# Performance work log

Measured on AMD Instinct MI355X. Metric: run time of the kernel, lower is better.

The kernel has to match this reference:

```python
import jax, jax.numpy as jnp
import numpy as np

B, S, D, H = 4, 2048, 768, 8
HD = D // H
EPS = 1e-5
NEG = -1e9


def setup_inputs() -> dict:
    key = jax.random.key(0)
    ks = jax.random.split(key, 12)
    s = 1.0 / np.sqrt(D)
    inp = {
        "hidden_states": jax.random.normal(ks[0], (B, S, D), dtype=jnp.float32),
        "anchor_mask": jax.random.bernoulli(ks[1], 0.5, (B, S)),
        "ln_g": jnp.ones((D,), jnp.float32),
        "ln_b": jnp.zeros((D,), jnp.float32),
        "Wq": jax.random.uniform(ks[2], (D, D), jnp.float32, -s, s),
        "bq": jax.random.uniform(ks[3], (D,), jnp.float32, -s, s),
        "Wk": jax.random.uniform(ks[4], (D, D), jnp.float32, -s, s),
        "bk": jax.random.uniform(ks[5], (D,), jnp.float32, -s, s),
        "Wv": jax.random.uniform(ks[6], (D, D), jnp.float32, -s, s),
        "bv": jax.random.uniform(ks[7], (D,), jnp.float32, -s, s),
        "Wo": jax.random.uniform(ks[8], (D, D), jnp.float32, -s, s),
        "bo": jax.random.uniform(ks[9], (D,), jnp.float32, -s, s),
    }
    return inp


def reference(hidden_states, anchor_mask, ln_g, ln_b, Wq, bq, Wk, bk, Wv, bv, Wo, bo):
    # LayerNorm (per-token, so applying to all tokens == applying to gathered anchors)
    mu = jnp.mean(hidden_states, axis=-1, keepdims=True)
    var = jnp.mean(jnp.square(hidden_states - mu), axis=-1, keepdims=True)
    x = (hidden_states - mu) * jax.lax.rsqrt(var + EPS) * ln_g + ln_b

    # QKV projections: torch Linear is x @ W.T + b
    q = (jnp.einsum('bsd,ed->bse', x, Wq) + bq).reshape(B, S, H, HD)
    k = (jnp.einsum('bsd,ed->bse', x, Wk) + bk).reshape(B, S, H, HD)
    v = (jnp.einsum('bsd,ed->bse', x, Wv) + bv).reshape(B, S, H, HD)

    scale = 1.0 / np.sqrt(HD)
    scores = jnp.einsum('bqhd,bkhd->bhqk', q, k) * scale
    # keys restricted to anchor positions (equivalent to the gather)
    key_mask = anchor_mask[:, None, None, :]  # (B,1,1,S)
    scores = jnp.where(key_mask, scores, NEG)
    attn = jax.nn.softmax(scores, axis=-1)  # dropout is identity in eval

    out = jnp.einsum('bhqk,bkhd->bqhd', attn, v).reshape(B, S, D)
    out = jnp.einsum('bsd,ed->bse', out, Wo) + bo
    # scatter back: zeros at non-anchor positions
    return out * anchor_mask[:, :, None].astype(out.dtype)
```

## Files before the change

kernel.cpp:

```cpp
#include <hip/hip_runtime.h>
#include <math.h>

#define S_LEN 2048
#define D_DIM 768
#define NH 8
#define HD 96
#define NTOK 8192

typedef short bf16x8 __attribute__((ext_vector_type(8)));
typedef float f32x4 __attribute__((ext_vector_type(4)));

__device__ __forceinline__ f32x4 mfma16(bf16x8 a, bf16x8 b, f32x4 c) {
    return __builtin_amdgcn_mfma_f32_16x16x32_bf16(a, b, c, 0, 0, 0);
}

__device__ __forceinline__ unsigned short f2bf(float f) {
    unsigned int u = __float_as_uint(f);
    u += 0x7fffu + ((u >> 16) & 1u);
    return (unsigned short)(u >> 16);
}

__device__ __forceinline__ void gl_lds16(const unsigned short* g, unsigned short* l) {
    __builtin_amdgcn_global_load_lds(
        (const __attribute__((address_space(1))) unsigned int*)g,
        (__attribute__((address_space(3))) unsigned int*)l, 16, 0, 0);
}

#define TILE_SHORTS 6144
#define BH_SHORTS   196608

__global__ __launch_bounds__(256) void prep_kernel(
    const unsigned char* __restrict__ mb, int* __restrict__ idx, int* __restrict__ cnt,
    const float* __restrict__ Wq, const float* __restrict__ Wk,
    const float* __restrict__ Wv, const float* __restrict__ Wo,
    unsigned short* __restrict__ W4b, float* __restrict__ out)
{
    const int bi = blockIdx.x;
    const int t  = threadIdx.x;

    if (bi < 4) {
        __shared__ int red[4];
        __shared__ int warp_tot[4];
        const int b = bi;
        int s = 0;
        for (int i = t; i < NTOK; i += 256) s += (int)mb[i];
        for (int off = 32; off > 0; off >>= 1) s += __shfl_down(s, off, 64);
        if ((t & 63) == 0) red[t >> 6] = s;
        __syncthreads();
        const int total = red[0] + red[1] + red[2] + red[3];
        const int mode = (total > 20000) ? 2 : ((total > 2500) ? 1 : 0);
        const int*   mi = (const int*)mb;
        const float* mf = (const float*)mb;
        const int p0 = t * 8;
        int av = 0, c = 0;
        #pragma unroll
        for (int j = 0; j < 8; ++j) {
            const int g = b * S_LEN + p0 + j;
            bool a;
            if (mode == 2)      a = (mf[g] != 0.0f);
            else if (mode == 1) a = (mb[g] != 0);
            else                a = (mi[g] != 0);
            if (a) { av |= (1 << j); ++c; }
        }
        const int lane = t & 63, w = t >> 6;
        int v = c;
        #pragma unroll
        for (int off = 1; off < 64; off <<= 1) {
            const int u = __shfl_up(v, off, 64);
            if (lane >= off) v += u;
        }
        if (lane == 63) warp_tot[w] = v;
        __syncthreads();
        int wbase = 0;
        for (int i = 0; i < w; ++i) wbase += warp_tot[i];
        int o = wbase + v - c;
        #pragma unroll
        for (int j = 0; j < 8; ++j)
            if (av & (1 << j)) idx[b * S_LEN + (o++)] = p0 + j;
        if (t == 255) cnt[b] = wbase + v;
    } else if (bi < 1156) {
        const int i = bi - 4;
        const int w = i / 288, blk = i % 288;
        const float* src = (w == 0) ? Wq : (w == 1) ? Wk : (w == 2) ? Wv : Wo;
        const int base = (blk * 256 + t) * 8;
        const float4 a = *(const float4*)&src[base];
        const float4 c = *(const float4*)&src[base + 4];
        uint4 u;
        u.x = (unsigned int)f2bf(a.x) | ((unsigned int)f2bf(a.y) << 16);
        u.y = (unsigned int)f2bf(a.z) | ((unsigned int)f2bf(a.w) << 16);
        u.z = (unsigned int)f2bf(c.x) | ((unsigned int)f2bf(c.y) << 16);
        u.w = (unsigned int)f2bf(c.z) | ((unsigned int)f2bf(c.w) << 16);
        *(uint4*)&W4b[(size_t)w * 589824 + base] = u;
    } else {
        const size_t i4 = (size_t)(bi - 1156) * 256 + t;
        float4 z; z.x = z.y = z.z = z.w = 0.0f;
        *(float4*)&out[i4 * 4] = z;
    }
}

__global__ __launch_bounds__(256) void ln_gather_kernel(
    const float* __restrict__ H, const float* __restrict__ g,
    const float* __restrict__ bta, const int* __restrict__ idx,
    const int* __restrict__ cnt, unsigned short* __restrict__ X)
{
    __shared__ float rs[4], rss[4];
    const int slot = blockIdx.x;
    const int b = slot >> 11, r = slot & (S_LEN - 1);
    if (r >= cnt[b]) return;
    const int p = idx[slot];
    const float* hr = H + (size_t)(b * S_LEN + p) * D_DIM;
    unsigned short* xr = X + (size_t)slot * D_DIM;
    const int t = threadIdx.x;
    const float v0 = hr[t], v1 = hr[t + 256], v2 = hr[t + 512];
    float s  = v0 + v1 + v2;
    float ss = v0*v0 + v1*v1 + v2*v2;
    for (int off = 32; off > 0; off >>= 1) {
        s  += __shfl_down(s,  off, 64);
        ss += __shfl_down(ss, off, 64);
    }
    if ((t & 63) == 0) { rs[t >> 6] = s; rss[t >> 6] = ss; }
    __syncthreads();
    const float sum = rs[0] + rs[1] + rs[2] + rs[3];
    const float sq  = rss[0] + rss[1] + rss[2] + rss[3];
    const float mu  = sum * (1.0f / D_DIM);
    const float var = sq * (1.0f / D_DIM) - mu * mu;
    const float rstd = rsqrtf(var + 1e-5f);
    xr[t]       = f2bf((v0 - mu) * rstd * g[t]       + bta[t]);
    xr[t + 256] = f2bf((v1 - mu) * rstd * g[t + 256] + bta[t + 256]);
    xr[t + 512] = f2bf((v2 - mu) * rstd * g[t + 512] + bta[t + 512]);
}

__global__ __launch_bounds__(256) void gemm_bf16(
    const unsigned short* __restrict__ A,
    const unsigned short* __restrict__ W4,
    const float* __restrict__ b0, const float* __restrict__ b1,
    const float* __restrict__ b2,
    const int* __restrict__ cnt, const int* __restrict__ idx,
    unsigned short* __restrict__ Qo, unsigned short* __restrict__ Kp,
    unsigned short* __restrict__ Vp, float* __restrict__ Fo,
    int oproj)
{
    const int z = blockIdx.z;
    const int m0 = blockIdx.y * 128;
    const int b  = m0 >> 11;
    const int rbase = m0 & (S_LEN - 1);
    const int nc = cnt[b];
    if (rbase >= nc) return;
    const int n0 = blockIdx.x * 128;
    const unsigned short* W = W4 + (size_t)z * 589824;
    const float* bias = (z == 0) ? b0 : (z == 1 ? b1 : b2);

    __shared__ unsigned short Al[128 * 32];
    __shared__ unsigned short Bl[128 * 32];

    const int t = threadIdx.x;
    const int srow = t >> 2, sg = t & 3;
    const int ra0 = b * S_LEN + min(rbase + srow,      nc - 1);
    const int ra1 = b * S_LEN + min(rbase + srow + 64, nc - 1);
    const unsigned short* gA0 = A + (size_t)ra0 * 768 + sg * 8;
    const unsigned short* gA1 = A + (size_t)ra1 * 768 + sg * 8;
    const unsigned short* gB0 = W + (size_t)(n0 + srow)      * 768 + sg * 8;
    const unsigned short* gB1 = W + (size_t)(n0 + srow + 64) * 768 + sg * 8;
    unsigned short* lA = Al + t * 8;
    unsigned short* lB = Bl + t * 8;

    const int w = t >> 6, lane = t & 63;
    const int l15 = lane & 15, quad = lane >> 4;
    const int mh = (w & 1) * 64, nh2 = (w >> 1) * 64;

    f32x4 acc[4][4] = {};

    int aoff[4], boff[4];
    #pragma unroll
    for (int i = 0; i < 4; ++i) {
        aoff[i] = (mh  + i * 16 + l15) * 32 + quad * 8;
        boff[i] = (nh2 + i * 16 + l15) * 32 + quad * 8;
    }

    for (int k0 = 0; k0 < 768; k0 += 32) {
        __syncthreads();
        gl_lds16(gA0 + k0, lA);
        gl_lds16(gA1 + k0, lA + 2048);
        gl_lds16(gB0 + k0, lB);
        gl_lds16(gB1 + k0, lB + 2048);
        __syncthreads();
        bf16x8 af[4], bfr[4];
        #pragma unroll
        for (int i = 0; i < 4; ++i) af[i]  = *(const bf16x8*)(Al + aoff[i]);
        #pragma unroll
        for (int i = 0; i < 4; ++i) bfr[i] = *(const bf16x8*)(Bl + boff[i]);
        #pragma unroll
        for (int ms = 0; ms < 4; ++ms)
            #pragma unroll
            for (int ns = 0; ns < 4; ++ns)
                acc[ms][ns] = mfma16(af[ms], bfr[ns], acc[ms][ns]);
    }

    if (!oproj) {
        if (z == 0) {
            #pragma unroll
            for (int ns = 0; ns < 4; ++ns) {
                const int n = n0 + nh2 + ns * 16 + l15;
                const float bv = bias[n];
                #pragma unroll
                for (int ms = 0; ms < 4; ++ms) {
                    const int ml = mh + ms * 16 + quad * 4;
                    #pragma unroll
                    for (int r = 0; r < 4; ++r) {
                        const int slot = b * S_LEN + rbase + ml + r;
                        Qo[(size_t)slot * 768 + n] = f2bf(acc[ms][ns][r] + bv);
                    }
                }
            }
        } else if (z == 1) {
            #pragma unroll
            for (int ns = 0; ns < 4; ++ns) {
                const int n = n0 + nh2 + ns * 16 + l15;
                const int h = n / 96, d = n - h * 96;
                const float bv = bias[n];
                unsigned short* base = Kp + (size_t)(b * 8 + h) * BH_SHORTS;
                const int dseg = d >> 3, dlo = d & 7;
                #pragma unroll
                for (int ms = 0; ms < 4; ++ms) {
                    const int ml = mh + ms * 16 + quad * 4;
                    #pragma unroll
                    for (int r = 0; r < 4; ++r) {
                        const int tok = rbase + ml + r;
                        const int kt = tok >> 6, tk = tok & 63;
                        const int g16 = tk >> 4, lr = tk & 15;
                        base[(size_t)kt * TILE_SHORTS +
                             (g16 * 192 + dseg * 16 + lr) * 8 + dlo] =
                            (tok < nc) ? f2bf(acc[ms][ns][r] + bv)
                                       : (unsigned short)0;
                    }
                }
            }
        } else {
            #pragma unroll
            for (int ns = 0; ns < 4; ++ns) {
                const int n = n0 + nh2 + ns * 16 + l15;
                const int h = n / 96, d = n - h * 96;
                const float bv = bias[n];
                unsigned short* base = Vp + (size_t)(b * 8 + h) * BH_SHORTS;
                const int dg = d >> 4, l16 = d & 15;
                #pragma unroll
                for (int ms = 0; ms < 4; ++ms) {
                    const int ml = mh + ms * 16 + quad * 4;
                    const int k = rbase + ml;
                    const int kt = k >> 6, tk = k & 63;
                    const int kseg = tk >> 3, klo = tk & 7;
                    const unsigned short h0 =
                        (k + 0 < nc) ? f2bf(acc[ms][ns][0] + bv) : (unsigned short)0;
                    const unsigned short h1 =
                        (k + 1 < nc) ? f2bf(acc[ms][ns][1] + bv) : (unsigned short)0;
                    const unsigned short h2 =
                        (k + 2 < nc) ? f2bf(acc[ms][ns][2] + bv) : (unsigned short)0;
                    const unsigned short h3 =
                        (k + 3 < nc) ? f2bf(acc[ms][ns][3] + bv) : (unsigned short)0;
                    uint2 u;
                    u.x = (unsigned int)h0 | ((unsigned int)h1 << 16);
                    u.y = (unsigned int)h2 | ((unsigned int)h3 << 16);
                    *(uint2*)&base[(size_t)kt * TILE_SHORTS +
                                   (dg * 128 + kseg * 16 + l16) * 8 + klo] = u;
                }
            }
        }
    } else {
        #pragma unroll
        for (int ns = 0; ns < 4; ++ns) {
            const int n = n0 + nh2 + ns * 16 + l15;
            const float bv = bias[n];
            #pragma unroll
            for (int ms = 0; ms < 4; ++ms) {
                const int ml = mh + ms * 16 + quad * 4;
                #pragma unroll
                for (int r = 0; r < 4; ++r) {
                    const int rloc = rbase + ml + r;
                    if (rloc < nc) {
                        const int orow = b * S_LEN + idx[b * S_LEN + rloc];
                        Fo[(size_t)orow * 768 + n] = acc[ms][ns][r] + bv;
                    }
                }
            }
        }
    }
}

__global__ __launch_bounds__(256) void attn_mfma(
    const unsigned short* __restrict__ Q,
    const unsigned short* __restrict__ Kp,
    const unsigned short* __restrict__ Vp,
    const int* __restrict__ cnt,
    unsigned short* __restrict__ O)
{
    const int bh = blockIdx.x & 31;
    const int b  = bh >> 3, h = bh & 7;
    const int q0 = (blockIdx.x >> 5) * 64;
    const int nk = cnt[b];
    if (q0 >= nk) return;

    __shared__ unsigned short SB[2 * 12288 + 4 * 1152];

    const int t = threadIdx.x, w = t >> 6, lane = t & 63;
    const int l15 = lane & 15, quad = lane >> 4;
    const int qw = q0 + w * 16;
    const int bS = b * S_LEN;
    const float CE = 0.14724459f;

    const int t8 = t * 8;
    const unsigned short* Kst = Kp + (size_t)(b * 8 + h) * BH_SHORTS + t8;
    const unsigned short* Vst = Vp + (size_t)(b * 8 + h) * BH_SHORTS + t8;

    const unsigned short* qrow = Q + (size_t)(bS + qw + l15) * 768 + h * 96 + quad * 8;
    bf16x8 qf[3];
    qf[0] = *(const bf16x8*)(qrow);
    qf[1] = *(const bf16x8*)(qrow + 32);
    qf[2] = *(const bf16x8*)(qrow + 64);

    unsigned short* Pw   = SB + 24576 + w * 1152;
    unsigned short* bufA = SB;
    unsigned short* bufB = SB + 12288;

    float lsum = 0.0f;
    f32x4 oacc[6] = {};

    const int kts = (nk + 63) >> 6;

    #pragma unroll
    for (int r = 0; r < 3; ++r) {
        gl_lds16(Kst + r * 2048, bufA + r * 2048 + t8);
        gl_lds16(Vst + r * 2048, bufA + 6144 + r * 2048 + t8);
    }
    Kst += TILE_SHORTS; Vst += TILE_SHORTS;
    __syncthreads();

    for (int kt = 0; kt < kts; ++kt) {
        if (kt + 1 < kts) {
            #pragma unroll
            for (int r = 0; r < 3; ++r) {
                gl_lds16(Kst + r * 2048, bufB + r * 2048 + t8);
                gl_lds16(Vst + r * 2048, bufB + 6144 + r * 2048 + t8);
            }
            Kst += TILE_SHORTS; Vst += TILE_SHORTS;
        }

        const unsigned short* Kl = bufA;
        const unsigned short* Vl = bufA + 6144;

        #pragma unroll
        for (int s = 0; s < 4; ++s) {
            f32x4 sa = {};
            __builtin_amdgcn_s_setprio(1);
            #pragma unroll
            for (int ks = 0; ks < 3; ++ks) {
                const bf16x8 kf = *(const bf16x8*)(Kl + (s * 192 + (quad + ks * 4) * 16 + l15) * 8);
                sa = mfma16(kf, qf[ks], sa);
            }
            __builtin_amdgcn_s_setprio(0);
            unsigned short pk[4];
            #pragma unroll
            for (int r = 0; r < 4; ++r) {
                const float p = exp2f(sa[r] * CE);
                lsum += p;
                pk[r] = f2bf(p);
            }
            uint2 u;
            u.x = (unsigned int)pk[0] | ((unsigned int)pk[1] << 16);
            u.y = (unsigned int)pk[2] | ((unsigned int)pk[3] << 16);
            *(uint2*)&Pw[l15 * 72 + s * 16 + quad * 4] = u;
        }

        const bf16x8 pb0 = *(const bf16x8*)(Pw + l15 * 72 + quad * 8);
        const bf16x8 pb1 = *(const bf16x8*)(Pw + l15 * 72 + 32 + quad * 8);

        __builtin_amdgcn_s_setprio(1);
        #pragma unroll
        for (int dt = 0; dt < 6; ++dt) {
            const bf16x8 v0f = *(const bf16x8*)(Vl + (dt * 128 + quad * 16 + l15) * 8);
            const bf16x8 v1f = *(const bf16x8*)(Vl + (dt * 128 + (quad + 4) * 16 + l15) * 8);
            oacc[dt] = mfma16(v0f, pb0, oacc[dt]);
            oacc[dt] = mfma16(v1f, pb1, oacc[dt]);
        }
        __builtin_amdgcn_s_setprio(0);

        __syncthreads();
        unsigned short* tmp = bufA; bufA = bufB; bufB = tmp;
    }

    lsum += __shfl_xor(lsum, 16);
    lsum += __shfl_xor(lsum, 32);
    lsum -= (float)((kts << 6) - nk);

    const int qi = qw + l15;
    if (qi < nk) {
        const float rl = 1.0f / lsum;
        unsigned short* og = O + (size_t)(bS + qi) * 768 + h * 96;
        #pragma unroll
        for (int dt = 0; dt < 6; ++dt) {
            const unsigned short o0 = f2bf(oacc[dt][0] * rl);
            const unsigned short o1 = f2bf(oacc[dt][1] * rl);
            const unsigned short o2 = f2bf(oacc[dt][2] * rl);
            const unsigned short o3 = f2bf(oacc[dt][3] * rl);
            uint2 u;
            u.x = (unsigned int)o0 | ((unsigned int)o1 << 16);
            u.y = (unsigned int)o2 | ((unsigned int)o3 << 16);
            *(uint2*)&og[dt * 16 + quad * 4] = u;
        }
    }
}

extern "C" void kernel_launch(void* const* d_in, const int* in_sizes, int n_in,
                              void* d_out, int out_size, void* d_ws, size_t ws_size,
                              hipStream_t stream)
{
    const float* hs  = (const float*)d_in[0];
    const unsigned char* am = (const unsigned char*)d_in[1];
    const float* lng = (const float*)d_in[2];
    const float* lnb = (const float*)d_in[3];
    const float* Wq  = (const float*)d_in[4];
    const float* bq  = (const float*)d_in[5];
    const float* Wk  = (const float*)d_in[6];
    const float* bk  = (const float*)d_in[7];
    const float* Wv  = (const float*)d_in[8];
    const float* bv  = (const float*)d_in[9];
    const float* Wo  = (const float*)d_in[10];
    const float* bo  = (const float*)d_in[11];

    char* ws = (char*)d_ws;
    const size_t BUF = (size_t)NTOK * 768 * 2;
    int* idx = (int*)ws;
    int* cnt = (int*)(ws + 32768);
    unsigned short* xb  = (unsigned short*)(ws + 65536);
    unsigned short* Qb  = (unsigned short*)(ws + 65536 + BUF);
    unsigned short* Kpb = (unsigned short*)(ws + 65536 + 2 * BUF);
    unsigned short* Vpb = (unsigned short*)(ws + 65536 + 3 * BUF);
    unsigned short* W4b = (unsigned short*)(ws + 65536 + 4 * BUF);
    unsigned short* Ob  = xb;
    float* out = (float*)d_out;

    prep_kernel<<<dim3(2692), dim3(256), 0, stream>>>(
        am, idx, cnt, Wq, Wk, Wv, Wo, W4b, out);

    ln_gather_kernel<<<dim3(NTOK), dim3(256), 0, stream>>>(hs, lng, lnb, idx, cnt, xb);

    gemm_bf16<<<dim3(6, 64, 3), dim3(256), 0, stream>>>(
        xb, W4b, bq, bk, bv, cnt, idx, Qb, Kpb, Vpb, nullptr, 0);

    attn_mfma<<<dim3(1024), dim3(256), 0, stream>>>(Qb, Kpb, Vpb, cnt, Ob);

    gemm_bf16<<<dim3(6, 64, 1), dim3(256), 0, stream>>>(
        Ob, W4b + (size_t)3 * 589824, bo, bo, bo, cnt, idx,
        nullptr, nullptr, nullptr, out, 1);
}
```

Baseline: 217.6 us.

## Switch attention to 32x32x16 MFMA with register-resident P via permlane32 swap

Rewrites the attention inner loop to use 32x32x16 bf16 MFMA tiles, with each wave now covering 32 queries and blocks shrunk to 128 threads (2 waves). The softmax probabilities are packed with v_cvt_pk_bf16_f32 and rearranged through permlane32_swap instead of going through an LDS staging buffer. This removes the per-tile LDS write/read round trip for P and the manual bf16 rounding. In exchange, each block has half as many threads sharing the same K/V LDS loads, which doubles the per-thread load count and changes occupancy.

Result: faster. 204.8 us (-5.9%).

```diff
diff --git a/kernel.cpp b/kernel.cpp
--- a/kernel.cpp
+++ b/kernel.cpp
@@ -9,15 +9,27 @@
 
 typedef short bf16x8 __attribute__((ext_vector_type(8)));
 typedef float f32x4 __attribute__((ext_vector_type(4)));
+typedef float f32x16 __attribute__((ext_vector_type(16)));
+typedef unsigned int u32x2 __attribute__((ext_vector_type(2)));
+typedef unsigned int u32x4 __attribute__((ext_vector_type(4)));
 
 __device__ __forceinline__ f32x4 mfma16(bf16x8 a, bf16x8 b, f32x4 c) {
     return __builtin_amdgcn_mfma_f32_16x16x32_bf16(a, b, c, 0, 0, 0);
+}
+__device__ __forceinline__ f32x16 mfma32(bf16x8 a, bf16x8 b, f32x16 c) {
+    return __builtin_amdgcn_mfma_f32_32x32x16_bf16(a, b, c, 0, 0, 0);
 }
 
 __device__ __forceinline__ unsigned short f2bf(float f) {
     unsigned int u = __float_as_uint(f);
     u += 0x7fffu + ((u >> 16) & 1u);
     return (unsigned short)(u >> 16);
+}
+
+__device__ __forceinline__ unsigned int cvtpk(float lo, float hi) {
+    unsigned int r;
+    asm("v_cvt_pk_bf16_f32 %0, %1, %2" : "=v"(r) : "v"(lo), "v"(hi));
+    return r;
 }
 
 __device__ __forceinline__ void gl_lds16(const unsigned short* g, unsigned short* l) {
@@ -286,7 +298,7 @@
     }
 }
 
-__global__ __launch_bounds__(256) void attn_mfma(
+__global__ __launch_bounds__(128) void attn_mfma(
     const unsigned short* __restrict__ Q,
     const unsigned short* __restrict__ Kp,
     const unsigned short* __restrict__ Vp,
@@ -299,37 +311,41 @@
     const int nk = cnt[b];
     if (q0 >= nk) return;
 
-    __shared__ unsigned short SB[2 * 12288 + 4 * 1152];
+    __shared__ unsigned short SB[2 * 12288];
 
     const int t = threadIdx.x, w = t >> 6, lane = t & 63;
-    const int l15 = lane & 15, quad = lane >> 4;
-    const int qw = q0 + w * 16;
-    const int bS = b * S_LEN;
+    const int l15 = lane & 15;
+    const int gh  = (lane >> 4) & 1;
+    const int hi  = lane >> 5;
+    const int q32 = lane & 31;
+    const int qw  = q0 + w * 32;
+    const int bS  = b * S_LEN;
     const float CE = 0.14724459f;
 
     const int t8 = t * 8;
     const unsigned short* Kst = Kp + (size_t)(b * 8 + h) * BH_SHORTS + t8;
     const unsigned short* Vst = Vp + (size_t)(b * 8 + h) * BH_SHORTS + t8;
 
-    const unsigned short* qrow = Q + (size_t)(bS + qw + l15) * 768 + h * 96 + quad * 8;
-    bf16x8 qf[3];
-    qf[0] = *(const bf16x8*)(qrow);
-    qf[1] = *(const bf16x8*)(qrow + 32);
-    qf[2] = *(const bf16x8*)(qrow + 64);
-
-    unsigned short* Pw   = SB + 24576 + w * 1152;
+    const unsigned short* qrow = Q + (size_t)(bS + qw + q32) * 768 + h * 96 + hi * 8;
+    bf16x8 qf[6];
+    #pragma unroll
+    for (int ks = 0; ks < 6; ++ks) qf[ks] = *(const bf16x8*)(qrow + ks * 16);
+
+    const int kb0 = (gh * 192 + hi * 16 + l15) * 8;
+    const int vb0 = (gh * 128 + hi * 16 + l15) * 8;
+
     unsigned short* bufA = SB;
     unsigned short* bufB = SB + 12288;
 
-    float lsum = 0.0f;
-    f32x4 oacc[6] = {};
+    float ls0 = 0.0f, ls1 = 0.0f;
+    f32x16 oacc[3] = {};
 
     const int kts = (nk + 63) >> 6;
 
     #pragma unroll
-    for (int r = 0; r < 3; ++r) {
-        gl_lds16(Kst + r * 2048, bufA + r * 2048 + t8);
-        gl_lds16(Vst + r * 2048, bufA + 6144 + r * 2048 + t8);
+    for (int r = 0; r < 6; ++r) {
+        gl_lds16(Kst + r * 1024, bufA + r * 1024 + t8);
+        gl_lds16(Vst + r * 1024, bufA + 6144 + r * 1024 + t8);
     }
     Kst += TILE_SHORTS; Vst += TILE_SHORTS;
     __syncthreads();
@@ -337,74 +353,76 @@
     for (int kt = 0; kt < kts; ++kt) {
         if (kt + 1 < kts) {
             #pragma unroll
-            for (int r = 0; r < 3; ++r) {
-                gl_lds16(Kst + r * 2048, bufB + r * 2048 + t8);
-                gl_lds16(Vst + r * 2048, bufB + 6144 + r * 2048 + t8);
+            for (int r = 0; r < 6; ++r) {
+                gl_lds16(Kst + r * 1024, bufB + r * 1024 + t8);
+                gl_lds16(Vst + r * 1024, bufB + 6144 + r * 1024 + t8);
             }
             Kst += TILE_SHORTS; Vst += TILE_SHORTS;
         }
-
         const unsigned short* Kl = bufA;
         const unsigned short* Vl = bufA + 6144;
 
         #pragma unroll
-        for (int s = 0; s < 4; ++s) {
-            f32x4 sa = {};
+        for (int s = 0; s < 2; ++s) {
+            f32x16 sa = {};
             __builtin_amdgcn_s_setprio(1);
             #pragma unroll
-            for (int ks = 0; ks < 3; ++ks) {
-                const bf16x8 kf = *(const bf16x8*)(Kl + (s * 192 + (quad + ks * 4) * 16 + l15) * 8);
-                sa = mfma16(kf, qf[ks], sa);
+            for (int ks = 0; ks < 6; ++ks) {
+                const bf16x8 kf = *(const bf16x8*)(Kl + kb0 + (s * 384 + ks * 32) * 8);
+                sa = mfma32(kf, qf[ks], sa);
             }
             __builtin_amdgcn_s_setprio(0);
-            unsigned short pk[4];
-            #pragma unroll
-            for (int r = 0; r < 4; ++r) {
-                const float p = exp2f(sa[r] * CE);
-                lsum += p;
-                pk[r] = f2bf(p);
-            }
-            uint2 u;
-            u.x = (unsigned int)pk[0] | ((unsigned int)pk[1] << 16);
-            u.y = (unsigned int)pk[2] | ((unsigned int)pk[3] << 16);
-            *(uint2*)&Pw[l15 * 72 + s * 16 + quad * 4] = u;
-        }
-
-        const bf16x8 pb0 = *(const bf16x8*)(Pw + l15 * 72 + quad * 8);
-        const bf16x8 pb1 = *(const bf16x8*)(Pw + l15 * 72 + 32 + quad * 8);
-
-        __builtin_amdgcn_s_setprio(1);
-        #pragma unroll
-        for (int dt = 0; dt < 6; ++dt) {
-            const bf16x8 v0f = *(const bf16x8*)(Vl + (dt * 128 + quad * 16 + l15) * 8);
-            const bf16x8 v1f = *(const bf16x8*)(Vl + (dt * 128 + (quad + 4) * 16 + l15) * 8);
-            oacc[dt] = mfma16(v0f, pb0, oacc[dt]);
-            oacc[dt] = mfma16(v1f, pb1, oacc[dt]);
-        }
-        __builtin_amdgcn_s_setprio(0);
+
+            unsigned int wv[8];
+            #pragma unroll
+            for (int j = 0; j < 8; ++j) {
+                const float e0 = exp2f(sa[2 * j]     * CE);
+                const float e1 = exp2f(sa[2 * j + 1] * CE);
+                if (j & 1) ls1 += e0 + e1; else ls0 += e0 + e1;
+                wv[j] = cvtpk(e0, e1);
+            }
+            const u32x2 r02 = __builtin_amdgcn_permlane32_swap(wv[0], wv[2], false, false);
+            const u32x2 r13 = __builtin_amdgcn_permlane32_swap(wv[1], wv[3], false, false);
+            const u32x2 r46 = __builtin_amdgcn_permlane32_swap(wv[4], wv[6], false, false);
+            const u32x2 r57 = __builtin_amdgcn_permlane32_swap(wv[5], wv[7], false, false);
+            const u32x4 pw0 = { r02.x, r13.x, r02.y, r13.y };
+            const u32x4 pw1 = { r46.x, r57.x, r46.y, r57.y };
+            const bf16x8 pb0 = __builtin_bit_cast(bf16x8, pw0);
+            const bf16x8 pb1 = __builtin_bit_cast(bf16x8, pw1);
+
+            const int kkb = s * 2;
+            __builtin_amdgcn_s_setprio(1);
+            #pragma unroll
+            for (int dg = 0; dg < 3; ++dg) {
+                const bf16x8 v0 = *(const bf16x8*)(Vl + vb0 + (dg * 256 + kkb * 32) * 8);
+                const bf16x8 v1 = *(const bf16x8*)(Vl + vb0 + (dg * 256 + (kkb + 1) * 32) * 8);
+                oacc[dg] = mfma32(v0, pb0, oacc[dg]);
+                oacc[dg] = mfma32(v1, pb1, oacc[dg]);
+            }
+            __builtin_amdgcn_s_setprio(0);
+        }
 
         __syncthreads();
         unsigned short* tmp = bufA; bufA = bufB; bufB = tmp;
     }
 
-    lsum += __shfl_xor(lsum, 16);
+    float lsum = ls0 + ls1;
     lsum += __shfl_xor(lsum, 32);
     lsum -= (float)((kts << 6) - nk);
 
-    const int qi = qw + l15;
+    const int qi = qw + q32;
     if (qi < nk) {
         const float rl = 1.0f / lsum;
         unsigned short* og = O + (size_t)(bS + qi) * 768 + h * 96;
         #pragma unroll
-        for (int dt = 0; dt < 6; ++dt) {
-            const unsigned short o0 = f2bf(oacc[dt][0] * rl);
-            const unsigned short o1 = f2bf(oacc[dt][1] * rl);
-            const unsigned short o2 = f2bf(oacc[dt][2] * rl);
-            const unsigned short o3 = f2bf(oacc[dt][3] * rl);
-            uint2 u;
-            u.x = (unsigned int)o0 | ((unsigned int)o1 << 16);
-            u.y = (unsigned int)o2 | ((unsigned int)o3 << 16);
-            *(uint2*)&og[dt * 16 + quad * 4] = u;
+        for (int dg = 0; dg < 3; ++dg) {
+            #pragma unroll
+            for (int m = 0; m < 4; ++m) {
+                uint2 u;
+                u.x = cvtpk(oacc[dg][4 * m]     * rl, oacc[dg][4 * m + 1] * rl);
+                u.y = cvtpk(oacc[dg][4 * m + 2] * rl, oacc[dg][4 * m + 3] * rl);
+                *(uint2*)&og[dg * 32 + m * 8 + hi * 4] = u;
+            }
         }
     }
 }
@@ -446,7 +464,7 @@
     gemm_bf16<<<dim3(6, 64, 3), dim3(256), 0, stream>>>(
         xb, W4b, bq, bk, bv, cnt, idx, Qb, Kpb, Vpb, nullptr, 0);
 
-    attn_mfma<<<dim3(1024), dim3(256), 0, stream>>>(Qb, Kpb, Vpb, cnt, Ob);
+    attn_mfma<<<dim3(1024), dim3(128), 0, stream>>>(Qb, Kpb, Vpb, cnt, Ob);
 
     gemm_bf16<<<dim3(6, 64, 1), dim3(256), 0, stream>>>(
         Ob, W4b + (size_t)3 * 589824, bo, bo, bo, cnt, idx,
```
